# Performance work log

Hardware: AMD Instinct MI355X
Metric: run time of the kernel (lower is better)

## Reference

```python
import jax, jax.numpy as jnp
import numpy as np

REG_M = 0.1     # reg_m_bregman
N_ITER = 30     # fixed MM iteration count (POT uses numItermax=1000 w/ early stop)
EPS = 1e-16     # POT's stabilizer added to the denominator


def setup_inputs() -> dict:
    key = jax.random.key(0)
    kx, ky = jax.random.split(key)
    x = jax.random.normal(kx, (4096, 256), dtype=jnp.float32)
    y = jax.random.normal(ky, (4096, 256), dtype=jnp.float32)
    # L2-normalize embeddings so squared distances lie in [0,4] and the
    # KL kernel exp(-M / (2*reg_m)) stays in a representable range.
    x = x / jnp.linalg.norm(x, axis=1, keepdims=True)
    y = y / jnp.linalg.norm(y, axis=1, keepdims=True)
    return {"x": x, "y": y}


def reference(x, y):
    m, n = x.shape[0], y.shape[0]
    # ot.dist default metric: squared euclidean  M[i,j] = ||x_i - y_j||^2
    M = (jnp.sum(x * x, axis=1)[:, None]
         + jnp.sum(y * y, axis=1)[None, :]
         - 2.0 * (x @ y.T))                                  # [m, n]
    a = jnp.full((m,), 1.0 / m, dtype=x.dtype)
    b = jnp.full((n,), 1.0 / n, dtype=x.dtype)
    # POT mm_unbalanced, div='kl', reg_m1=reg_m2=reg_m, reg=0:
    # r1 = r2 = 1/2, K = sqrt(a_i b_j) * exp(-M / (2*reg_m)), G0 = a (x) b,
    # G <- K * G / (sqrt(rowsum_i) * sqrt(colsum_j) + eps)
    K = jnp.sqrt(a[:, None] * b[None, :]) * jnp.exp(-M / (2.0 * REG_M))
    G0 = a[:, None] * b[None, :]

    def step(G, _):
        Gd = jnp.sqrt(G.sum(axis=1)[:, None] * G.sum(axis=0)[None, :]) + EPS
        return K * G / Gd, None

    Pi, _ = jax.lax.scan(step, G0, None, length=N_ITER)
    # (Pi @ M.T).mean() = sum_j (sum_i Pi[i,j]) * (sum_k M[k,j]) / m^2
    return jnp.dot(Pi.sum(axis=0), M.sum(axis=0)) / (m * m)
```

## Files before the change

kernel.cpp:

```cpp
#include <hip/hip_runtime.h>
#include <math.h>

#define MDIM 4096
#define NDIM 4096
#define DDIM 256
#define N_ITER 30

#define TWO_KAPPA 14.426950408889634
#define CLCONST  (-12.0 - TWO_KAPPA)

typedef __attribute__((ext_vector_type(8))) short bf16x8;
typedef __attribute__((ext_vector_type(4))) float f32x4;

__device__ __forceinline__ unsigned encf(float f) {
  unsigned u = __float_as_uint(f);
  return (u & 0x80000000u) ? ~u : (u | 0x80000000u);
}
__device__ __forceinline__ float decf(unsigned u) {
  return __uint_as_float((u & 0x80000000u) ? (u ^ 0x80000000u) : ~u);
}

#define AL_RLX(p)      __hip_atomic_load((p), __ATOMIC_RELAXED, __HIP_MEMORY_SCOPE_AGENT)
#define AS_RLX(p, v)   __hip_atomic_store((p), (v), __ATOMIC_RELAXED, __HIP_MEMORY_SCOPE_AGENT)
#define AADD_RLX(p, v) __hip_atomic_fetch_add((p), (v), __ATOMIC_RELAXED, __HIP_MEMORY_SCOPE_AGENT)
#define AMAX_RLX(p, v) __hip_atomic_fetch_max((p), (v), __ATOMIC_RELAXED, __HIP_MEMORY_SCOPE_AGENT)

__global__ void norms_kernel(const float* __restrict__ x, const float* __restrict__ y,
                             float* __restrict__ xx, float* __restrict__ yy,
                             float* __restrict__ Sxx) {
  int wid = threadIdx.x >> 6, lane = threadIdx.x & 63;
  int row = blockIdx.x * 4 + wid;
  const float* src = (row < MDIM) ? x : y;
  int r = (row < MDIM) ? row : row - MDIM;
  const float4* p = (const float4*)(src + (size_t)r * DDIM);
  float4 v = p[lane];
  float s = v.x*v.x + v.y*v.y + v.z*v.z + v.w*v.w;
  #pragma unroll
  for (int off = 32; off; off >>= 1) s += __shfl_down(s, off);
  if (lane == 0) {
    if (row < MDIM) { xx[r] = s; atomicAdd(Sxx, s); }
    else            { yy[r] = s; }
  }
}

__global__ void sx_kernel(const float* __restrict__ x, float* __restrict__ sx) {
  int tx = threadIdx.x;
  int r0 = blockIdx.x * 16;
  float s = 0.f;
  #pragma unroll
  for (int r = 0; r < 16; ++r) s += x[(size_t)(r0 + r) * DDIM + tx];
  atomicAdd(&sx[tx], s);
}

__global__ void colM_kernel(const float* __restrict__ y, const float* __restrict__ sx,
                            const float* __restrict__ yy, const float* __restrict__ Sxx,
                            float* __restrict__ colM) {
  int wid = threadIdx.x >> 6, lane = threadIdx.x & 63;
  int j = blockIdx.x * 4 + wid;
  const float4* py = (const float4*)(y + (size_t)j * DDIM);
  const float4* ps = (const float4*)sx;
  float4 a = py[lane], b = ps[lane];
  float s = a.x*b.x + a.y*b.y + a.z*b.z + a.w*b.w;
  #pragma unroll
  for (int off = 32; off; off >>= 1) s += __shfl_down(s, off);
  if (lane == 0) colM[j] = *Sxx + (float)MDIM * yy[j] - 2.f * s;
}

__global__ void split_kernel(const float* __restrict__ x, const float* __restrict__ y,
                             ushort* __restrict__ xh, ushort* __restrict__ xl,
                             ushort* __restrict__ yh, ushort* __restrict__ yl) {
  int g = blockIdx.x * 256 + threadIdx.x;
  int e; const float4* src; ushort* dh; ushort* dl;
  if (g < 262144) { e = g;          src = (const float4*)x; dh = xh; dl = xl; }
  else            { e = g - 262144; src = (const float4*)y; dh = yh; dl = yl; }
  float4 v = src[e];
  float f[4] = {v.x, v.y, v.z, v.w};
  ushort hs[4], ls[4];
  #pragma unroll
  for (int i = 0; i < 4; ++i) {
    unsigned u = __float_as_uint(f[i]);
    unsigned hr = (u + 0x7FFFu + ((u >> 16) & 1u)) >> 16;
    hs[i] = (ushort)hr;
    float hf = __uint_as_float(hr << 16);
    float lo = f[i] - hf;
    unsigned ul = __float_as_uint(lo);
    unsigned lr = (ul + 0x7FFFu + ((ul >> 16) & 1u)) >> 16;
    ls[i] = (ushort)lr;
  }
  *(ushort4*)(dh + (size_t)e * 4) = make_ushort4(hs[0], hs[1], hs[2], hs[3]);
  *(ushort4*)(dl + (size_t)e * 4) = make_ushort4(ls[0], ls[1], ls[2], ls[3]);
}

#define GPAD 56
__global__ __launch_bounds__(256)
void gemm_mfma_kernel(const ushort* __restrict__ xh, const ushort* __restrict__ xl,
                      const ushort* __restrict__ yh, const ushort* __restrict__ yl,
                      short* __restrict__ D16, float* __restrict__ maxdot) {
  __shared__ ushort As[2][128][GPAD];
  __shared__ ushort Bs[2][128][GPAD];
  int tid = threadIdx.x;
  int lane = tid & 63, wid = tid >> 6;
  int bm = blockIdx.x & 31, bn = blockIdx.x >> 5;
  int wrow = (wid >> 1) * 64, wcol = (wid & 1) * 64;
  f32x4 acc[4][4] = {};

  int c0 = tid, c1 = tid + 256;
  int r0 = c0 >> 2, k80 = (c0 & 3) * 8;
  int r1 = c1 >> 2, k81 = (c1 & 3) * 8;
  const size_t arow0 = (size_t)(bm * 128 + r0) * DDIM;
  const size_t arow1 = (size_t)(bm * 128 + r1) * DDIM;
  const size_t brow0 = (size_t)(bn * 128 + r0) * DDIM;
  const size_t brow1 = (size_t)(bn * 128 + r1) * DDIM;

  for (int k0 = 0; k0 < DDIM; k0 += 32) {
    *(uint4*)&As[0][r0][k80] = *(const uint4*)(xh + arow0 + k0 + k80);
    *(uint4*)&As[0][r1][k81] = *(const uint4*)(xh + arow1 + k0 + k81);
    *(uint4*)&As[1][r0][k80] = *(const uint4*)(xl + arow0 + k0 + k80);
    *(uint4*)&As[1][r1][k81] = *(const uint4*)(xl + arow1 + k0 + k81);
    *(uint4*)&Bs[0][r0][k80] = *(const uint4*)(yh + brow0 + k0 + k80);
    *(uint4*)&Bs[0][r1][k81] = *(const uint4*)(yh + brow1 + k0 + k81);
    *(uint4*)&Bs[1][r0][k80] = *(const uint4*)(yl + brow0 + k0 + k80);
    *(uint4*)&Bs[1][r1][k81] = *(const uint4*)(yl + brow1 + k0 + k81);
    __syncthreads();
    int fr = lane & 15, kg = lane >> 4;
    bf16x8 ah[4], al[4], bh[4], bl[4];
    #pragma unroll
    for (int i = 0; i < 4; ++i) {
      ah[i] = *(const bf16x8*)&As[0][wrow + i * 16 + fr][kg * 8];
      al[i] = *(const bf16x8*)&As[1][wrow + i * 16 + fr][kg * 8];
      bh[i] = *(const bf16x8*)&Bs[0][wcol + i * 16 + fr][kg * 8];
      bl[i] = *(const bf16x8*)&Bs[1][wcol + i * 16 + fr][kg * 8];
    }
    #pragma unroll
    for (int i = 0; i < 4; ++i)
      #pragma unroll
      for (int j = 0; j < 4; ++j) {
        acc[i][j] = __builtin_amdgcn_mfma_f32_16x16x32_bf16(ah[i], bh[j], acc[i][j], 0, 0, 0);
        acc[i][j] = __builtin_amdgcn_mfma_f32_16x16x32_bf16(ah[i], bl[j], acc[i][j], 0, 0, 0);
        acc[i][j] = __builtin_amdgcn_mfma_f32_16x16x32_bf16(al[i], bh[j], acc[i][j], 0, 0, 0);
      }
    __syncthreads();
  }
  float tmax = -1.f;
  #pragma unroll
  for (int i = 0; i < 4; ++i) {
    #pragma unroll
    for (int j = 0; j < 4; ++j) {
      int col = bn * 128 + wcol + j * 16 + (lane & 15);
      #pragma unroll
      for (int r = 0; r < 4; ++r) {
        float d = acc[i][j][r];
        tmax = fmaxf(tmax, d);
        int q = __float2int_rn(fminf(fmaxf(d * 65536.f, -32767.f), 32767.f));
        int row = bm * 128 + wrow + i * 16 + (lane >> 4) * 4 + r;
        D16[(size_t)row * NDIM + col] = (short)q;
      }
    }
  }
  __shared__ float sm[4];
  #pragma unroll
  for (int off = 32; off; off >>= 1) tmax = fmaxf(tmax, __shfl_down(tmax, off));
  if (lane == 0) sm[wid] = tmax;
  __syncthreads();
  if (tid == 0) {
    float m = fmaxf(fmaxf(sm[0], sm[1]), fmaxf(sm[2], sm[3]));
    atomicMax((int*)maxdot, __float_as_int(fmaxf(m, 0.f)));
  }
}

__global__ __launch_bounds__(1024)
void solve_kernel(const short* __restrict__ D16,
                  float* __restrict__ colp,
                  float* __restrict__ psi_pub,
                  const float* __restrict__ maxdot,
                  unsigned* phimaxS, unsigned* psimaxS,
                  unsigned* flag1, unsigned* flag2,
                  const float* __restrict__ colM,
                  float* lossacc, unsigned* lossdone,
                  float* __restrict__ out) {
  __shared__ ushort stripeS[16 * 4096];
  __shared__ float  vecS[4096];
  __shared__ float  redrow[16][16];
  __shared__ float  red2[16][16];
  __shared__ float  ownS[16];
  __shared__ float  sS[2];
  int tid = threadIdx.x, lane = tid & 63, wid = tid >> 6;
  int b = blockIdx.x;
  float md = maxdot[0];

  {
    const uint4* src = (const uint4*)(D16 + (size_t)b * 16 * NDIM);
    uint4* dst = (uint4*)stripeS;
    #pragma unroll
    for (int k = 0; k < 8; ++k) dst[tid + 1024 * k] = src[tid + 1024 * k];
  }
  if (tid < 16) ownS[tid] = -6.f;
  __syncthreads();

  for (int t = 1; t <= N_ITER; ++t) {
    float sD  = (float)((double)t * (TWO_KAPPA / 65536.0));
    float tCL = (float)((double)t * CLCONST);
    float s2k = (float)((double)t * TWO_KAPPA);

    if (t > 1) {
      if (tid == 0) {
        while (AL_RLX(&flag2[(t - 1) * 16]) < 256u) __builtin_amdgcn_s_sleep(2);
        unsigned uf = 0, up = 0;
        #pragma unroll
        for (int s = 0; s < 16; ++s) {
          unsigned a = AL_RLX(&phimaxS[t * 16 + s]); uf = a > uf ? a : uf;
          unsigned c = AL_RLX(&psimaxS[t * 16 + s]); up = c > up ? c : up;
        }
        sS[0] = decf(uf); sS[1] = decf(up);
      }
      __syncthreads();
    }
    float fm = (t == 1) ? -6.f : sS[0];
    float pm = (t == 1) ? -6.f : sS[1];
    float tLmax = fmaf(s2k, md, tCL);
    float S  = tLmax + fm + pm - 100.f;
    float WS = tCL - S;

    if (t == 1) {
      *(float4*)&vecS[4 * tid] = make_float4(-6.f, -6.f, -6.f, -6.f);
    } else {
      const unsigned long long* sp =
          (const unsigned long long*)(psi_pub + (size_t)(t & 1) * 4096 + 4 * tid);
      unsigned long long a = AL_RLX(sp), c = AL_RLX(sp + 1);
      float4 v;
      v.x = __uint_as_float((unsigned)a); v.y = __uint_as_float((unsigned)(a >> 32));
      v.z = __uint_as_float((unsigned)c); v.w = __uint_as_float((unsigned)(c >> 32));
      *(float4*)&vecS[4 * tid] = v;
    }
    __syncthreads();

    float4 psi4 = *(const float4*)&vecS[4 * tid];
    float P0 = psi4.x + WS, P1 = psi4.y + WS, P2 = psi4.z + WS, P3 = psi4.w + WS;
    float c0 = 0.f, c1 = 0.f, c2 = 0.f, c3 = 0.f;
    float rs[16];
    #pragma unroll
    for (int r = 0; r < 16; ++r) {
      float phr = ownS[r];
      int2 dv = *(const int2*)(stripeS + r * 4096 + 4 * tid);
      float d0 = (float)((short)(dv.x & 0xFFFF));
      float d1 = (float)(dv.x >> 16);
      float d2 = (float)((short)(dv.y & 0xFFFF));
      float d3 = (float)(dv.y >> 16);
      float e0 = exp2f(fmaf(d0, sD, P0 + phr));
      float e1 = exp2f(fmaf(d1, sD, P1 + phr));
      float e2 = exp2f(fmaf(d2, sD, P2 + phr));
      float e3 = exp2f(fmaf(d3, sD, P3 + phr));
      c0 += e0; c1 += e1; c2 += e2; c3 += e3;
      rs[r] = (e0 + e1) + (e2 + e3);
    }
    {
      unsigned long long u0 = ((unsigned long long)__float_as_uint(c1) << 32) | __float_as_uint(c0);
      unsigned long long u1 = ((unsigned long long)__float_as_uint(c3) << 32) | __float_as_uint(c2);
      unsigned long long* cp = (unsigned long long*)(colp + (size_t)b * 4096 + 4 * tid);
      AS_RLX(cp, u0); AS_RLX(cp + 1, u1);
    }
    if (t < N_ITER) {
      #pragma unroll
      for (int r = 0; r < 16; ++r) {
        float v = rs[r];
        #pragma unroll
        for (int o = 32; o; o >>= 1) v += __shfl_down(v, o);
        if (lane == 0) redrow[r][wid] = v;
      }
      __syncthreads();
      if (tid < 16) {
        float s = 0.f;
        #pragma unroll
        for (int w = 0; w < 16; ++w) s += redrow[tid][w];
        float pn = ownS[tid] - 0.5f * (S + log2f(fmaxf(s, 1e-30f)));
        ownS[tid] = pn;
        float mx = pn;
        #pragma unroll
        for (int o = 8; o; o >>= 1) mx = fmaxf(mx, __shfl_down(mx, o));
        if (tid == 0) AMAX_RLX(&phimaxS[(t + 1) * 16 + (b & 15)], encf(mx));
      }
    }
    asm volatile("s_waitcnt vmcnt(0)" ::: "memory");
    __syncthreads();
    if (tid == 0) {
      AADD_RLX(&flag1[t * 16], 1u);
      while (AL_RLX(&flag1[t * 16]) < 256u) __builtin_amdgcn_s_sleep(2);
    }
    __syncthreads();

    {
      int k  = tid >> 2;
      int cq = (tid & 3) * 4;
      const unsigned long long* rp =
          (const unsigned long long*)(colp + (size_t)k * 4096 + 16 * b + cq);
      unsigned long long a = AL_RLX(rp), c = AL_RLX(rp + 1);
      float f0 = __uint_as_float((unsigned)a), f1 = __uint_as_float((unsigned)(a >> 32));
      float f2 = __uint_as_float((unsigned)c), f3 = __uint_as_float((unsigned)(c >> 32));
      #pragma unroll
      for (int o = 4; o < 64; o <<= 1) {
        f0 += __shfl_down(f0, o); f1 += __shfl_down(f1, o);
        f2 += __shfl_down(f2, o); f3 += __shfl_down(f3, o);
      }
      if (lane < 4) *(float4*)&red2[wid][lane * 4] = make_float4(f0, f1, f2, f3);
    }
    __syncthreads();
    if (tid < 16) {
      float tot = 0.f;
      #pragma unroll
      for (int w = 0; w < 16; ++w) tot += red2[w][tid];
      int jj = 16 * b + tid;
      if (t < N_ITER) {
        float pn = vecS[jj] - 0.5f * (S + log2f(fmaxf(tot, 1e-30f)));
        AS_RLX(&psi_pub[(size_t)((t + 1) & 1) * 4096 + jj], pn);
        float mx = pn;
        #pragma unroll
        for (int o = 8; o; o >>= 1) mx = fmaxf(mx, __shfl_down(mx, o));
        if (tid == 0) {
          AMAX_RLX(&psimaxS[(t + 1) * 16 + (b & 15)], encf(mx));
          asm volatile("s_waitcnt vmcnt(0)" ::: "memory");
          AADD_RLX(&flag2[t * 16], 1u);
        }
      } else {
        float term = (tot * 9.094947017729282e-13f) * colM[jj];
        #pragma unroll
        for (int o = 8; o; o >>= 1) term += __shfl_down(term, o);
        if (tid == 0) {
          AADD_RLX(&lossacc[b & 15], term);
          asm volatile("s_waitcnt vmcnt(0)" ::: "memory");
          AADD_RLX(lossdone, 1u);
          if (b == 0) {
            while (AL_RLX(lossdone) < 256u) __builtin_amdgcn_s_sleep(2);
            float tt = 0.f;
            #pragma unroll
            for (int s = 0; s < 16; ++s) tt += AL_RLX(&lossacc[s]);
            out[0] = exp2f(log2f(tt) + S + 16.f);
          }
        }
      }
    }
  }
}

extern "C" void kernel_launch(void* const* d_in, const int* in_sizes, int n_in,
                              void* d_out, int out_size, void* d_ws, size_t ws_size,
                              hipStream_t stream) {
  const float* x = (const float*)d_in[0];
  const float* y = (const float*)d_in[1];
  float* out = (float*)d_out;

  char* ws = (char*)d_ws;
  size_t off = 0;
  auto alloc = [&](size_t bytes) -> void* {
    void* p = ws + off;
    off += (bytes + 255) & ~(size_t)255;
    return p;
  };
  short*    D16     = (short*)alloc((size_t)MDIM * NDIM * 2);
  float*    colp    = (float*)alloc((size_t)256 * NDIM * 4);
  ushort*   xh      = (ushort*)alloc((size_t)MDIM * DDIM * 2);
  ushort*   xl      = (ushort*)alloc((size_t)MDIM * DDIM * 2);
  ushort*   yh      = (ushort*)alloc((size_t)NDIM * DDIM * 2);
  ushort*   yl      = (ushort*)alloc((size_t)NDIM * DDIM * 2);
  float*    xx      = (float*)alloc(MDIM * 4);
  float*    yy      = (float*)alloc(NDIM * 4);
  float*    sx      = (float*)alloc(DDIM * 4);
  float*    colM    = (float*)alloc(NDIM * 4);
  float*    Sxx     = (float*)alloc(4);
  float*    maxd    = (float*)alloc(4);
  float*    psi_pub = (float*)alloc(2 * NDIM * 4);
  unsigned* phimaxS = (unsigned*)alloc(32 * 16 * 4);
  unsigned* psimaxS = (unsigned*)alloc(32 * 16 * 4);
  unsigned* flag1   = (unsigned*)alloc(32 * 16 * 4);
  unsigned* flag2   = (unsigned*)alloc(32 * 16 * 4);
  float*    lossacc = (float*)alloc(16 * 4);
  unsigned* lossdone= (unsigned*)alloc(16 * 4);

  hipMemsetAsync(Sxx, 0, 4, stream);
  hipMemsetAsync(maxd, 0, 4, stream);
  hipMemsetAsync(sx, 0, DDIM * 4, stream);
  hipMemsetAsync(phimaxS, 0, 32 * 16 * 4, stream);
  hipMemsetAsync(psimaxS, 0, 32 * 16 * 4, stream);
  hipMemsetAsync(flag1, 0, 32 * 16 * 4, stream);
  hipMemsetAsync(flag2, 0, 32 * 16 * 4, stream);
  hipMemsetAsync(lossacc, 0, 16 * 4, stream);
  hipMemsetAsync(lossdone, 0, 16 * 4, stream);

  norms_kernel<<<2048, 256, 0, stream>>>(x, y, xx, yy, Sxx);
  sx_kernel<<<256, 256, 0, stream>>>(x, sx);
  colM_kernel<<<1024, 256, 0, stream>>>(y, sx, yy, Sxx, colM);
  split_kernel<<<2048, 256, 0, stream>>>(x, y, xh, xl, yh, yl);
  gemm_mfma_kernel<<<1024, 256, 0, stream>>>(xh, xl, yh, yl, D16, maxd);

  void* kargs[] = {(void*)&D16, (void*)&colp, (void*)&psi_pub,
                   (void*)&maxd, (void*)&phimaxS, (void*)&psimaxS,
                   (void*)&flag1, (void*)&flag2,
                   (void*)&colM, (void*)&lossacc, (void*)&lossdone,
                   (void*)&out};
  hipLaunchCooperativeKernel((void*)solve_kernel, dim3(256), dim3(1024),
                             kargs, 0, stream);
}
```

Before: 989.4 us.

## Replace two-barrier column exchange with atomic column sums and redundant psi update

Each block now atomically adds its column partial sums into four per-iteration accumulators instead of writing a per-block partial row. After one hierarchical arrival barrier, every block reads the full column sums and recomputes psi and its maximum locally, instead of a second grid barrier that reduces and redistributes psi. This drops one grid-wide barrier per iteration and the psi publish round-trip. In exchange it issues many float atomics per iteration, every block repeats the psi update, and the buffer sized per iteration must be zeroed with a memset each launch.

```diff
diff --git a/kernel.cpp b/kernel.cpp
--- a/kernel.cpp
+++ b/kernel.cpp
@@ -21,7 +21,6 @@
 }
 
 #define AL_RLX(p)      __hip_atomic_load((p), __ATOMIC_RELAXED, __HIP_MEMORY_SCOPE_AGENT)
-#define AS_RLX(p, v)   __hip_atomic_store((p), (v), __ATOMIC_RELAXED, __HIP_MEMORY_SCOPE_AGENT)
 #define AADD_RLX(p, v) __hip_atomic_fetch_add((p), (v), __ATOMIC_RELAXED, __HIP_MEMORY_SCOPE_AGENT)
 #define AMAX_RLX(p, v) __hip_atomic_fetch_max((p), (v), __ATOMIC_RELAXED, __HIP_MEMORY_SCOPE_AGENT)
 
@@ -170,22 +169,21 @@
 
 __global__ __launch_bounds__(1024)
 void solve_kernel(const short* __restrict__ D16,
-                  float* __restrict__ colp,
-                  float* __restrict__ psi_pub,
+                  float* __restrict__ colq,
                   const float* __restrict__ maxdot,
-                  unsigned* phimaxS, unsigned* psimaxS,
-                  unsigned* flag1, unsigned* flag2,
+                  unsigned* __restrict__ phimaxS,
+                  unsigned* __restrict__ arrS,
+                  unsigned* __restrict__ rootA,
                   const float* __restrict__ colM,
-                  float* lossacc, unsigned* lossdone,
                   float* __restrict__ out) {
   __shared__ ushort stripeS[16 * 4096];
-  __shared__ float  vecS[4096];
   __shared__ float  redrow[16][16];
-  __shared__ float  red2[16][16];
+  __shared__ float  redm[16];
   __shared__ float  ownS[16];
-  __shared__ float  sS[2];
+  __shared__ float  sS[1];
   int tid = threadIdx.x, lane = tid & 63, wid = tid >> 6;
   int b = blockIdx.x;
+  int g = b & 3;
   float md = maxdot[0];
 
   {
@@ -195,47 +193,19 @@
     for (int k = 0; k < 8; ++k) dst[tid + 1024 * k] = src[tid + 1024 * k];
   }
   if (tid < 16) ownS[tid] = -6.f;
+  float4 psi4 = make_float4(-6.f, -6.f, -6.f, -6.f);
+  float phimax = -6.f, psimax = -6.f;
   __syncthreads();
 
   for (int t = 1; t <= N_ITER; ++t) {
     float sD  = (float)((double)t * (TWO_KAPPA / 65536.0));
     float tCL = (float)((double)t * CLCONST);
     float s2k = (float)((double)t * TWO_KAPPA);
-
-    if (t > 1) {
-      if (tid == 0) {
-        while (AL_RLX(&flag2[(t - 1) * 16]) < 256u) __builtin_amdgcn_s_sleep(2);
-        unsigned uf = 0, up = 0;
-        #pragma unroll
-        for (int s = 0; s < 16; ++s) {
-          unsigned a = AL_RLX(&phimaxS[t * 16 + s]); uf = a > uf ? a : uf;
-          unsigned c = AL_RLX(&psimaxS[t * 16 + s]); up = c > up ? c : up;
-        }
-        sS[0] = decf(uf); sS[1] = decf(up);
-      }
-      __syncthreads();
-    }
-    float fm = (t == 1) ? -6.f : sS[0];
-    float pm = (t == 1) ? -6.f : sS[1];
     float tLmax = fmaf(s2k, md, tCL);
-    float S  = tLmax + fm + pm - 100.f;
+    float S  = tLmax + phimax + psimax - 100.f;
     float WS = tCL - S;
-
-    if (t == 1) {
-      *(float4*)&vecS[4 * tid] = make_float4(-6.f, -6.f, -6.f, -6.f);
-    } else {
-      const unsigned long long* sp =
-          (const unsigned long long*)(psi_pub + (size_t)(t & 1) * 4096 + 4 * tid);
-      unsigned long long a = AL_RLX(sp), c = AL_RLX(sp + 1);
-      float4 v;
-      v.x = __uint_as_float((unsigned)a); v.y = __uint_as_float((unsigned)(a >> 32));
-      v.z = __uint_as_float((unsigned)c); v.w = __uint_as_float((unsigned)(c >> 32));
-      *(float4*)&vecS[4 * tid] = v;
-    }
-    __syncthreads();
-
-    float4 psi4 = *(const float4*)&vecS[4 * tid];
     float P0 = psi4.x + WS, P1 = psi4.y + WS, P2 = psi4.z + WS, P3 = psi4.w + WS;
+
     float c0 = 0.f, c1 = 0.f, c2 = 0.f, c3 = 0.f;
     float rs[16];
     #pragma unroll
@@ -254,10 +224,11 @@
       rs[r] = (e0 + e1) + (e2 + e3);
     }
     {
-      unsigned long long u0 = ((unsigned long long)__float_as_uint(c1) << 32) | __float_as_uint(c0);
-      unsigned long long u1 = ((unsigned long long)__float_as_uint(c3) << 32) | __float_as_uint(c2);
-      unsigned long long* cp = (unsigned long long*)(colp + (size_t)b * 4096 + 4 * tid);
-      AS_RLX(cp, u0); AS_RLX(cp + 1, u1);
+      float* cq = colq + ((size_t)(t - 1) * 4 + g) * 4096 + 4 * tid;
+      AADD_RLX(cq + 0, c0);
+      AADD_RLX(cq + 1, c1);
+      AADD_RLX(cq + 2, c2);
+      AADD_RLX(cq + 3, c3);
     }
     if (t < N_ITER) {
       #pragma unroll
@@ -283,58 +254,76 @@
     asm volatile("s_waitcnt vmcnt(0)" ::: "memory");
     __syncthreads();
     if (tid == 0) {
-      AADD_RLX(&flag1[t * 16], 1u);
-      while (AL_RLX(&flag1[t * 16]) < 256u) __builtin_amdgcn_s_sleep(2);
-    }
-    __syncthreads();
-
-    {
-      int k  = tid >> 2;
-      int cq = (tid & 3) * 4;
-      const unsigned long long* rp =
-          (const unsigned long long*)(colp + (size_t)k * 4096 + 16 * b + cq);
-      unsigned long long a = AL_RLX(rp), c = AL_RLX(rp + 1);
-      float f0 = __uint_as_float((unsigned)a), f1 = __uint_as_float((unsigned)(a >> 32));
-      float f2 = __uint_as_float((unsigned)c), f3 = __uint_as_float((unsigned)(c >> 32));
-      #pragma unroll
-      for (int o = 4; o < 64; o <<= 1) {
-        f0 += __shfl_down(f0, o); f1 += __shfl_down(f1, o);
-        f2 += __shfl_down(f2, o); f3 += __shfl_down(f3, o);
-      }
-      if (lane < 4) *(float4*)&red2[wid][lane * 4] = make_float4(f0, f1, f2, f3);
-    }
-    __syncthreads();
-    if (tid < 16) {
-      float tot = 0.f;
-      #pragma unroll
-      for (int w = 0; w < 16; ++w) tot += red2[w][tid];
-      int jj = 16 * b + tid;
-      if (t < N_ITER) {
-        float pn = vecS[jj] - 0.5f * (S + log2f(fmaxf(tot, 1e-30f)));
-        AS_RLX(&psi_pub[(size_t)((t + 1) & 1) * 4096 + jj], pn);
-        float mx = pn;
-        #pragma unroll
-        for (int o = 8; o; o >>= 1) mx = fmaxf(mx, __shfl_down(mx, o));
+      unsigned old = AADD_RLX(&arrS[t * 16 + (b & 15)], 1u);
+      if (old == 15u) AADD_RLX(&rootA[t * 16], 1u);
+    }
+
+    if (t < N_ITER) {
+      if (tid == 0) {
+        while (AL_RLX(&rootA[t * 16]) < 16u) __builtin_amdgcn_s_sleep(4);
+        unsigned uf = 0;
+        #pragma unroll
+        for (int s = 0; s < 16; ++s) {
+          unsigned a = AL_RLX(&phimaxS[(t + 1) * 16 + s]);
+          uf = a > uf ? a : uf;
+        }
+        sS[0] = decf(uf);
+      }
+      __syncthreads();
+      {
+        const float* cr = colq + (size_t)(t - 1) * 4 * 4096;
+        float4 q0 = *(const float4*)(cr + 0 * 4096 + 4 * tid);
+        float4 q1 = *(const float4*)(cr + 1 * 4096 + 4 * tid);
+        float4 q2 = *(const float4*)(cr + 2 * 4096 + 4 * tid);
+        float4 q3 = *(const float4*)(cr + 3 * 4096 + 4 * tid);
+        float t0 = (q0.x + q1.x) + (q2.x + q3.x);
+        float t1 = (q0.y + q1.y) + (q2.y + q3.y);
+        float t2 = (q0.z + q1.z) + (q2.z + q3.z);
+        float t3 = (q0.w + q1.w) + (q2.w + q3.w);
+        psi4.x -= 0.5f * (S + log2f(fmaxf(t0, 1e-30f)));
+        psi4.y -= 0.5f * (S + log2f(fmaxf(t1, 1e-30f)));
+        psi4.z -= 0.5f * (S + log2f(fmaxf(t2, 1e-30f)));
+        psi4.w -= 0.5f * (S + log2f(fmaxf(t3, 1e-30f)));
+        float mx = fmaxf(fmaxf(psi4.x, psi4.y), fmaxf(psi4.z, psi4.w));
+        #pragma unroll
+        for (int o = 32; o; o >>= 1) mx = fmaxf(mx, __shfl_down(mx, o));
+        if (lane == 0) redm[wid] = mx;
+      }
+      __syncthreads();
+      {
+        float pm = redm[0];
+        #pragma unroll
+        for (int w = 1; w < 16; ++w) pm = fmaxf(pm, redm[w]);
+        psimax = pm;
+        phimax = sS[0];
+      }
+      __syncthreads();
+    } else {
+      if (b == 0) {
         if (tid == 0) {
-          AMAX_RLX(&psimaxS[(t + 1) * 16 + (b & 15)], encf(mx));
-          asm volatile("s_waitcnt vmcnt(0)" ::: "memory");
-          AADD_RLX(&flag2[t * 16], 1u);
+          while (AL_RLX(&rootA[t * 16]) < 16u) __builtin_amdgcn_s_sleep(4);
         }
-      } else {
-        float term = (tot * 9.094947017729282e-13f) * colM[jj];
-        #pragma unroll
-        for (int o = 8; o; o >>= 1) term += __shfl_down(term, o);
+        __syncthreads();
+        const float* cr = colq + (size_t)(t - 1) * 4 * 4096;
+        float4 q0 = *(const float4*)(cr + 0 * 4096 + 4 * tid);
+        float4 q1 = *(const float4*)(cr + 1 * 4096 + 4 * tid);
+        float4 q2 = *(const float4*)(cr + 2 * 4096 + 4 * tid);
+        float4 q3 = *(const float4*)(cr + 3 * 4096 + 4 * tid);
+        float4 mv = *(const float4*)(colM + 4 * tid);
+        const float sc = 9.094947017729282e-13f;
+        float term = ((q0.x + q1.x) + (q2.x + q3.x)) * sc * mv.x
+                   + ((q0.y + q1.y) + (q2.y + q3.y)) * sc * mv.y
+                   + ((q0.z + q1.z) + (q2.z + q3.z)) * sc * mv.z
+                   + ((q0.w + q1.w) + (q2.w + q3.w)) * sc * mv.w;
+        #pragma unroll
+        for (int o = 32; o; o >>= 1) term += __shfl_down(term, o);
+        if (lane == 0) redm[wid] = term;
+        __syncthreads();
         if (tid == 0) {
-          AADD_RLX(&lossacc[b & 15], term);
-          asm volatile("s_waitcnt vmcnt(0)" ::: "memory");
-          AADD_RLX(lossdone, 1u);
-          if (b == 0) {
-            while (AL_RLX(lossdone) < 256u) __builtin_amdgcn_s_sleep(2);
-            float tt = 0.f;
-            #pragma unroll
-            for (int s = 0; s < 16; ++s) tt += AL_RLX(&lossacc[s]);
-            out[0] = exp2f(log2f(tt) + S + 16.f);
-          }
+          float tot = 0.f;
+          #pragma unroll
+          for (int w = 0; w < 16; ++w) tot += redm[w];
+          out[0] = exp2f(log2f(tot) + S + 16.f);
         }
       }
     }
@@ -356,7 +345,7 @@
     return p;
   };
   short*    D16     = (short*)alloc((size_t)MDIM * NDIM * 2);
-  float*    colp    = (float*)alloc((size_t)256 * NDIM * 4);
+  float*    colq    = (float*)alloc((size_t)N_ITER * 4 * NDIM * 4);
   ushort*   xh      = (ushort*)alloc((size_t)MDIM * DDIM * 2);
   ushort*   xl      = (ushort*)alloc((size_t)MDIM * DDIM * 2);
   ushort*   yh      = (ushort*)alloc((size_t)NDIM * DDIM * 2);
@@ -367,23 +356,17 @@
   float*    colM    = (float*)alloc(NDIM * 4);
   float*    Sxx     = (float*)alloc(4);
   float*    maxd    = (float*)alloc(4);
-  float*    psi_pub = (float*)alloc(2 * NDIM * 4);
   unsigned* phimaxS = (unsigned*)alloc(32 * 16 * 4);
-  unsigned* psimaxS = (unsigned*)alloc(32 * 16 * 4);
-  unsigned* flag1   = (unsigned*)alloc(32 * 16 * 4);
-  unsigned* flag2   = (unsigned*)alloc(32 * 16 * 4);
-  float*    lossacc = (float*)alloc(16 * 4);
-  unsigned* lossdone= (unsigned*)alloc(16 * 4);
+  unsigned* arrS    = (unsigned*)alloc(32 * 16 * 4);
+  unsigned* rootA   = (unsigned*)alloc(32 * 16 * 4);
 
   hipMemsetAsync(Sxx, 0, 4, stream);
   hipMemsetAsync(maxd, 0, 4, stream);
   hipMemsetAsync(sx, 0, DDIM * 4, stream);
+  hipMemsetAsync(colq, 0, (size_t)N_ITER * 4 * NDIM * 4, stream);
   hipMemsetAsync(phimaxS, 0, 32 * 16 * 4, stream);
-  hipMemsetAsync(psimaxS, 0, 32 * 16 * 4, stream);
-  hipMemsetAsync(flag1, 0, 32 * 16 * 4, stream);
-  hipMemsetAsync(flag2, 0, 32 * 16 * 4, stream);
-  hipMemsetAsync(lossacc, 0, 16 * 4, stream);
-  hipMemsetAsync(lossdone, 0, 16 * 4, stream);
+  hipMemsetAsync(arrS, 0, 32 * 16 * 4, stream);
+  hipMemsetAsync(rootA, 0, 32 * 16 * 4, stream);
 
   norms_kernel<<<2048, 256, 0, stream>>>(x, y, xx, yy, Sxx);
   sx_kernel<<<256, 256, 0, stream>>>(x, sx);
@@ -391,11 +374,9 @@
   split_kernel<<<2048, 256, 0, stream>>>(x, y, xh, xl, yh, yl);
   gemm_mfma_kernel<<<1024, 256, 0, stream>>>(xh, xl, yh, yl, D16, maxd);
 
-  void* kargs[] = {(void*)&D16, (void*)&colp, (void*)&psi_pub,
-                   (void*)&maxd, (void*)&phimaxS, (void*)&psimaxS,
-                   (void*)&flag1, (void*)&flag2,
-                   (void*)&colM, (void*)&lossacc, (void*)&lossdone,
-                   (void*)&out};
+  void* kargs[] = {(void*)&D16, (void*)&colq, (void*)&maxd,
+                   (void*)&phimaxS, (void*)&arrS, (void*)&rootA,
+                   (void*)&colM, (void*)&out};
   hipLaunchCooperativeKernel((void*)solve_kernel, dim3(256), dim3(1024),
                              kargs, 0, stream);
 }
```

New measurement: 1.149 ms. +16.1%, slower.

## Partition solve matrix into 256x256 tiles and use hierarchical grid barriers

Applied to the files above, without the earlier changes.

Each block now owns a 256x256 tile of the quantized distance matrix instead of a 16-row stripe. Row and column partial sums are each reduced across only 16 blocks, which shrinks the column-partial traffic from 256x4096 floats to 16x4096 and lets phi and psi be updated in the same phase. The flat 256-way atomic barriers become two-level arrive counters (16 groups feeding a root). The cost is more scattered partial-sum writes and reads per block, plus still two grid barriers per iteration with a more involved synchronisation protocol.

```diff
diff --git a/kernel.cpp b/kernel.cpp
--- a/kernel.cpp
+++ b/kernel.cpp
@@ -11,6 +11,7 @@
 
 typedef __attribute__((ext_vector_type(8))) short bf16x8;
 typedef __attribute__((ext_vector_type(4))) float f32x4;
+typedef unsigned long long ull;
 
 __device__ __forceinline__ unsigned encf(float f) {
   unsigned u = __float_as_uint(f);
@@ -170,78 +171,58 @@
 
 __global__ __launch_bounds__(1024)
 void solve_kernel(const short* __restrict__ D16,
-                  float* __restrict__ colp,
-                  float* __restrict__ psi_pub,
+                  float* __restrict__ rp, float* __restrict__ cp,
+                  float* __restrict__ pubPhi, float* __restrict__ pubPsi,
                   const float* __restrict__ maxdot,
-                  unsigned* phimaxS, unsigned* psimaxS,
-                  unsigned* flag1, unsigned* flag2,
+                  unsigned* __restrict__ phimaxS, unsigned* __restrict__ psimaxS,
+                  unsigned* __restrict__ arrA, unsigned* __restrict__ rootA,
+                  unsigned* __restrict__ arrB, unsigned* __restrict__ rootB,
                   const float* __restrict__ colM,
-                  float* lossacc, unsigned* lossdone,
+                  float* __restrict__ lossacc, unsigned* __restrict__ lossdone,
                   float* __restrict__ out) {
-  __shared__ ushort stripeS[16 * 4096];
-  __shared__ float  vecS[4096];
-  __shared__ float  redrow[16][16];
-  __shared__ float  red2[16][16];
-  __shared__ float  ownS[16];
+  __shared__ ushort tileS[256 * 256];
+  __shared__ float  cpS[16][256];
+  __shared__ float  phiS[256], psiS[256];
   __shared__ float  sS[2];
-  int tid = threadIdx.x, lane = tid & 63, wid = tid >> 6;
+  int tid = threadIdx.x, lane = tid & 63;
   int b = blockIdx.x;
+  int R = b >> 4, C = b & 15;
+  int rg = tid >> 6, c4 = tid & 63;
   float md = maxdot[0];
 
   {
-    const uint4* src = (const uint4*)(D16 + (size_t)b * 16 * NDIM);
-    uint4* dst = (uint4*)stripeS;
+    int row = tid >> 2, chunk = tid & 3;
+    const ushort* src = (const ushort*)D16 + (size_t)(256 * R + row) * NDIM + 256 * C + 64 * chunk;
+    ushort* dst = tileS + row * 256 + 64 * chunk;
     #pragma unroll
-    for (int k = 0; k < 8; ++k) dst[tid + 1024 * k] = src[tid + 1024 * k];
-  }
-  if (tid < 16) ownS[tid] = -6.f;
+    for (int q = 0; q < 8; ++q)
+      *(uint4*)(dst + 8 * q) = *(const uint4*)(src + 8 * q);
+  }
+  float ownPhi = -6.f, ownPsi = -6.f;
+  float phimax = -6.f, psimax = -6.f;
+  if (tid < 256) { phiS[tid] = -6.f; psiS[tid] = -6.f; }
   __syncthreads();
 
+  float S = 0.f;
   for (int t = 1; t <= N_ITER; ++t) {
     float sD  = (float)((double)t * (TWO_KAPPA / 65536.0));
     float tCL = (float)((double)t * CLCONST);
     float s2k = (float)((double)t * TWO_KAPPA);
-
-    if (t > 1) {
-      if (tid == 0) {
-        while (AL_RLX(&flag2[(t - 1) * 16]) < 256u) __builtin_amdgcn_s_sleep(2);
-        unsigned uf = 0, up = 0;
-        #pragma unroll
-        for (int s = 0; s < 16; ++s) {
-          unsigned a = AL_RLX(&phimaxS[t * 16 + s]); uf = a > uf ? a : uf;
-          unsigned c = AL_RLX(&psimaxS[t * 16 + s]); up = c > up ? c : up;
-        }
-        sS[0] = decf(uf); sS[1] = decf(up);
-      }
-      __syncthreads();
-    }
-    float fm = (t == 1) ? -6.f : sS[0];
-    float pm = (t == 1) ? -6.f : sS[1];
     float tLmax = fmaf(s2k, md, tCL);
-    float S  = tLmax + fm + pm - 100.f;
+    S = tLmax + phimax + psimax - 100.f;
     float WS = tCL - S;
 
-    if (t == 1) {
-      *(float4*)&vecS[4 * tid] = make_float4(-6.f, -6.f, -6.f, -6.f);
-    } else {
-      const unsigned long long* sp =
-          (const unsigned long long*)(psi_pub + (size_t)(t & 1) * 4096 + 4 * tid);
-      unsigned long long a = AL_RLX(sp), c = AL_RLX(sp + 1);
-      float4 v;
-      v.x = __uint_as_float((unsigned)a); v.y = __uint_as_float((unsigned)(a >> 32));
-      v.z = __uint_as_float((unsigned)c); v.w = __uint_as_float((unsigned)(c >> 32));
-      *(float4*)&vecS[4 * tid] = v;
-    }
-    __syncthreads();
-
-    float4 psi4 = *(const float4*)&vecS[4 * tid];
-    float P0 = psi4.x + WS, P1 = psi4.y + WS, P2 = psi4.z + WS, P3 = psi4.w + WS;
-    float c0 = 0.f, c1 = 0.f, c2 = 0.f, c3 = 0.f;
+    float P0 = psiS[c4 * 4 + 0] + WS;
+    float P1 = psiS[c4 * 4 + 1] + WS;
+    float P2 = psiS[c4 * 4 + 2] + WS;
+    float P3 = psiS[c4 * 4 + 3] + WS;
+
+    float ca0 = 0.f, ca1 = 0.f, ca2 = 0.f, ca3 = 0.f;
     float rs[16];
     #pragma unroll
     for (int r = 0; r < 16; ++r) {
-      float phr = ownS[r];
-      int2 dv = *(const int2*)(stripeS + r * 4096 + 4 * tid);
+      float phr = phiS[rg * 16 + r];
+      int2 dv = *(const int2*)(tileS + (rg * 16 + r) * 256 + c4 * 4);
       float d0 = (float)((short)(dv.x & 0xFFFF));
       float d1 = (float)(dv.x >> 16);
       float d2 = (float)((short)(dv.y & 0xFFFF));
@@ -250,14 +231,8 @@
       float e1 = exp2f(fmaf(d1, sD, P1 + phr));
       float e2 = exp2f(fmaf(d2, sD, P2 + phr));
       float e3 = exp2f(fmaf(d3, sD, P3 + phr));
-      c0 += e0; c1 += e1; c2 += e2; c3 += e3;
+      ca0 += e0; ca1 += e1; ca2 += e2; ca3 += e3;
       rs[r] = (e0 + e1) + (e2 + e3);
-    }
-    {
-      unsigned long long u0 = ((unsigned long long)__float_as_uint(c1) << 32) | __float_as_uint(c0);
-      unsigned long long u1 = ((unsigned long long)__float_as_uint(c3) << 32) | __float_as_uint(c2);
-      unsigned long long* cp = (unsigned long long*)(colp + (size_t)b * 4096 + 4 * tid);
-      AS_RLX(cp, u0); AS_RLX(cp + 1, u1);
     }
     if (t < N_ITER) {
       #pragma unroll
@@ -265,63 +240,81 @@
         float v = rs[r];
         #pragma unroll
         for (int o = 32; o; o >>= 1) v += __shfl_down(v, o);
-        if (lane == 0) redrow[r][wid] = v;
-      }
-      __syncthreads();
-      if (tid < 16) {
-        float s = 0.f;
-        #pragma unroll
-        for (int w = 0; w < 16; ++w) s += redrow[tid][w];
-        float pn = ownS[tid] - 0.5f * (S + log2f(fmaxf(s, 1e-30f)));
-        ownS[tid] = pn;
-        float mx = pn;
-        #pragma unroll
-        for (int o = 8; o; o >>= 1) mx = fmaxf(mx, __shfl_down(mx, o));
-        if (tid == 0) AMAX_RLX(&phimaxS[(t + 1) * 16 + (b & 15)], encf(mx));
-      }
+        if (lane == 0) AS_RLX(&rp[C * 4096 + 256 * R + rg * 16 + r], v);
+      }
+    }
+    cpS[rg][c4 * 4 + 0] = ca0; cpS[rg][c4 * 4 + 1] = ca1;
+    cpS[rg][c4 * 4 + 2] = ca2; cpS[rg][c4 * 4 + 3] = ca3;
+    __syncthreads();
+    if (tid < 256) {
+      float tot = 0.f;
+      #pragma unroll
+      for (int g2 = 0; g2 < 16; ++g2) tot += cpS[g2][tid];
+      AS_RLX(&cp[R * 4096 + 256 * C + tid], tot);
     }
     asm volatile("s_waitcnt vmcnt(0)" ::: "memory");
     __syncthreads();
     if (tid == 0) {
-      AADD_RLX(&flag1[t * 16], 1u);
-      while (AL_RLX(&flag1[t * 16]) < 256u) __builtin_amdgcn_s_sleep(2);
+      unsigned old = AADD_RLX(&arrA[t * 16 + (b & 15)], 1u);
+      if (old == 15u) AADD_RLX(&rootA[t * 16], 1u);
+      while (AL_RLX(&rootA[t * 16]) < 16u) __builtin_amdgcn_s_sleep(2);
     }
     __syncthreads();
 
-    {
-      int k  = tid >> 2;
-      int cq = (tid & 3) * 4;
-      const unsigned long long* rp =
-          (const unsigned long long*)(colp + (size_t)k * 4096 + 16 * b + cq);
-      unsigned long long a = AL_RLX(rp), c = AL_RLX(rp + 1);
-      float f0 = __uint_as_float((unsigned)a), f1 = __uint_as_float((unsigned)(a >> 32));
-      float f2 = __uint_as_float((unsigned)c), f3 = __uint_as_float((unsigned)(c >> 32));
-      #pragma unroll
-      for (int o = 4; o < 64; o <<= 1) {
-        f0 += __shfl_down(f0, o); f1 += __shfl_down(f1, o);
-        f2 += __shfl_down(f2, o); f3 += __shfl_down(f3, o);
-      }
-      if (lane < 4) *(float4*)&red2[wid][lane * 4] = make_float4(f0, f1, f2, f3);
-    }
-    __syncthreads();
-    if (tid < 16) {
-      float tot = 0.f;
-      #pragma unroll
-      for (int w = 0; w < 16; ++w) tot += red2[w][tid];
-      int jj = 16 * b + tid;
-      if (t < N_ITER) {
-        float pn = vecS[jj] - 0.5f * (S + log2f(fmaxf(tot, 1e-30f)));
-        AS_RLX(&psi_pub[(size_t)((t + 1) & 1) * 4096 + jj], pn);
-        float mx = pn;
-        #pragma unroll
-        for (int o = 8; o; o >>= 1) mx = fmaxf(mx, __shfl_down(mx, o));
+    if (t < N_ITER) {
+      if (tid < 16) {
+        float s1 = 0.f, s2 = 0.f;
+        #pragma unroll
+        for (int k = 0; k < 16; ++k) {
+          s1 += AL_RLX(&rp[k * 4096 + 16 * b + tid]);
+          s2 += AL_RLX(&cp[k * 4096 + 16 * b + tid]);
+        }
+        float pnf = ownPhi - 0.5f * (S + log2f(fmaxf(s1, 1e-30f)));
+        float pns = ownPsi - 0.5f * (S + log2f(fmaxf(s2, 1e-30f)));
+        ownPhi = pnf; ownPsi = pns;
+        AS_RLX(&pubPhi[16 * b + tid], pnf);
+        AS_RLX(&pubPsi[16 * b + tid], pns);
+        float mf = pnf, ms = pns;
+        #pragma unroll
+        for (int o = 8; o; o >>= 1) {
+          mf = fmaxf(mf, __shfl_down(mf, o));
+          ms = fmaxf(ms, __shfl_down(ms, o));
+        }
         if (tid == 0) {
-          AMAX_RLX(&psimaxS[(t + 1) * 16 + (b & 15)], encf(mx));
-          asm volatile("s_waitcnt vmcnt(0)" ::: "memory");
-          AADD_RLX(&flag2[t * 16], 1u);
+          AMAX_RLX(&phimaxS[(t + 1) * 16 + (b & 15)], encf(mf));
+          AMAX_RLX(&psimaxS[(t + 1) * 16 + (b & 15)], encf(ms));
         }
-      } else {
-        float term = (tot * 9.094947017729282e-13f) * colM[jj];
+      }
+      if (tid == 0) {
+        asm volatile("s_waitcnt vmcnt(0)" ::: "memory");
+        unsigned old = AADD_RLX(&arrB[t * 16 + (b & 15)], 1u);
+        if (old == 15u) AADD_RLX(&rootB[t * 16], 1u);
+        while (AL_RLX(&rootB[t * 16]) < 16u) __builtin_amdgcn_s_sleep(2);
+        unsigned uf = 0, up = 0;
+        #pragma unroll
+        for (int s = 0; s < 16; ++s) {
+          unsigned a  = AL_RLX(&phimaxS[(t + 1) * 16 + s]); uf = a  > uf ? a  : uf;
+          unsigned c2 = AL_RLX(&psimaxS[(t + 1) * 16 + s]); up = c2 > up ? c2 : up;
+        }
+        sS[0] = decf(uf); sS[1] = decf(up);
+      }
+      __syncthreads();
+      phimax = sS[0]; psimax = sS[1];
+      if (tid < 128) {
+        ull a = AL_RLX((const ull*)&pubPhi[256 * R + 2 * tid]);
+        phiS[2 * tid]     = __uint_as_float((unsigned)a);
+        phiS[2 * tid + 1] = __uint_as_float((unsigned)(a >> 32));
+        ull c2 = AL_RLX((const ull*)&pubPsi[256 * C + 2 * tid]);
+        psiS[2 * tid]     = __uint_as_float((unsigned)c2);
+        psiS[2 * tid + 1] = __uint_as_float((unsigned)(c2 >> 32));
+      }
+      __syncthreads();
+    } else {
+      if (tid < 16) {
+        float s2 = 0.f;
+        #pragma unroll
+        for (int k = 0; k < 16; ++k) s2 += AL_RLX(&cp[k * 4096 + 16 * b + tid]);
+        float term = (s2 * 9.094947017729282e-13f) * colM[16 * b + tid];
         #pragma unroll
         for (int o = 8; o; o >>= 1) term += __shfl_down(term, o);
         if (tid == 0) {
@@ -356,7 +349,8 @@
     return p;
   };
   short*    D16     = (short*)alloc((size_t)MDIM * NDIM * 2);
-  float*    colp    = (float*)alloc((size_t)256 * NDIM * 4);
+  float*    rp      = (float*)alloc((size_t)16 * NDIM * 4);
+  float*    cp      = (float*)alloc((size_t)16 * NDIM * 4);
   ushort*   xh      = (ushort*)alloc((size_t)MDIM * DDIM * 2);
   ushort*   xl      = (ushort*)alloc((size_t)MDIM * DDIM * 2);
   ushort*   yh      = (ushort*)alloc((size_t)NDIM * DDIM * 2);
@@ -367,11 +361,14 @@
   float*    colM    = (float*)alloc(NDIM * 4);
   float*    Sxx     = (float*)alloc(4);
   float*    maxd    = (float*)alloc(4);
-  float*    psi_pub = (float*)alloc(2 * NDIM * 4);
+  float*    pubPhi  = (float*)alloc(MDIM * 4);
+  float*    pubPsi  = (float*)alloc(NDIM * 4);
   unsigned* phimaxS = (unsigned*)alloc(32 * 16 * 4);
   unsigned* psimaxS = (unsigned*)alloc(32 * 16 * 4);
-  unsigned* flag1   = (unsigned*)alloc(32 * 16 * 4);
-  unsigned* flag2   = (unsigned*)alloc(32 * 16 * 4);
+  unsigned* arrA    = (unsigned*)alloc(32 * 16 * 4);
+  unsigned* rootA   = (unsigned*)alloc(32 * 16 * 4);
+  unsigned* arrB    = (unsigned*)alloc(32 * 16 * 4);
+  unsigned* rootB   = (unsigned*)alloc(32 * 16 * 4);
   float*    lossacc = (float*)alloc(16 * 4);
   unsigned* lossdone= (unsigned*)alloc(16 * 4);
 
@@ -380,8 +377,10 @@
   hipMemsetAsync(sx, 0, DDIM * 4, stream);
   hipMemsetAsync(phimaxS, 0, 32 * 16 * 4, stream);
   hipMemsetAsync(psimaxS, 0, 32 * 16 * 4, stream);
-  hipMemsetAsync(flag1, 0, 32 * 16 * 4, stream);
-  hipMemsetAsync(flag2, 0, 32 * 16 * 4, stream);
+  hipMemsetAsync(arrA, 0, 32 * 16 * 4, stream);
+  hipMemsetAsync(rootA, 0, 32 * 16 * 4, stream);
+  hipMemsetAsync(arrB, 0, 32 * 16 * 4, stream);
+  hipMemsetAsync(rootB, 0, 32 * 16 * 4, stream);
   hipMemsetAsync(lossacc, 0, 16 * 4, stream);
   hipMemsetAsync(lossdone, 0, 16 * 4, stream);
 
@@ -391,11 +390,11 @@
   split_kernel<<<2048, 256, 0, stream>>>(x, y, xh, xl, yh, yl);
   gemm_mfma_kernel<<<1024, 256, 0, stream>>>(xh, xl, yh, yl, D16, maxd);
 
-  void* kargs[] = {(void*)&D16, (void*)&colp, (void*)&psi_pub,
-                   (void*)&maxd, (void*)&phimaxS, (void*)&psimaxS,
-                   (void*)&flag1, (void*)&flag2,
-                   (void*)&colM, (void*)&lossacc, (void*)&lossdone,
-                   (void*)&out};
+  void* kargs[] = {(void*)&D16, (void*)&rp, (void*)&cp,
+                   (void*)&pubPhi, (void*)&pubPsi, (void*)&maxd,
+                   (void*)&phimaxS, (void*)&psimaxS,
+                   (void*)&arrA, (void*)&rootA, (void*)&arrB, (void*)&rootB,
+                   (void*)&colM, (void*)&lossacc, (void*)&lossdone, (void*)&out};
   hipLaunchCooperativeKernel((void*)solve_kernel, dim3(256), dim3(1024),
                              kargs, 0, stream);
 }
```

New measurement: 1.063 ms. 7.4% more time.
